# Optimization experiments

Hardware: AMD Instinct MI355X
Metric: run time of the kernel (lower is better)

The kernel has to match this reference:

```python
import jax, jax.numpy as jnp
import numpy as np

B, T, DIM, H = 4, 1024, 2048, 16
HD = DIM // H  # head_dim = 128


def _rope_tables(t, hd, theta=10000.0):
    freqs = 1.0 / (theta ** (np.arange(0, hd, 2, dtype=np.float32) / hd))  # [hd/2]
    ang = np.outer(np.arange(t, dtype=np.float32), freqs)  # [T, hd/2]
    return jnp.asarray(np.cos(ang)), jnp.asarray(np.sin(ang))


def setup_inputs() -> dict:
    key = jax.random.key(0)
    ks = jax.random.split(key, 5)
    x = jax.random.normal(ks[0], (B, T, DIM), dtype=jnp.float32)
    s = 1.0 / np.sqrt(DIM)
    wq = jax.random.normal(ks[1], (DIM, DIM), dtype=jnp.float32) * s
    wk = jax.random.normal(ks[2], (DIM, DIM), dtype=jnp.float32) * s
    wv = jax.random.normal(ks[3], (DIM, DIM), dtype=jnp.float32) * s
    wo = jax.random.normal(ks[4], (DIM, DIM), dtype=jnp.float32) * s
    freqs_cos, freqs_sin = _rope_tables(T, HD)
    return {"x": x, "freqs_cos": freqs_cos, "freqs_sin": freqs_sin,
            "wq": wq, "wk": wk, "wv": wv, "wo": wo}


def _apply_rope(t, cos, sin):
    # t: [B,T,H,HD]; cos/sin: [T,HD/2]. Adjacent feature pairs form complex numbers.
    tr = t.reshape(*t.shape[:-1], HD // 2, 2)
    te, to = tr[..., 0], tr[..., 1]
    c = cos[None, :, None, :]
    s = sin[None, :, None, :]
    oe = te * c - to * s
    oo = te * s + to * c
    return jnp.stack([oe, oo], axis=-1).reshape(t.shape)


def reference(x, freqs_cos, freqs_sin, wq, wk, wv, wo):
    # Linear layers: y = x @ W^T (torch nn.Linear convention)
    q = (x @ wq.T).reshape(B, T, H, HD)
    k = (x @ wk.T).reshape(B, T, H, HD)
    v = (x @ wv.T).reshape(B, T, H, HD)
    q = _apply_rope(q, freqs_cos, freqs_sin)
    k = _apply_rope(k, freqs_cos, freqs_sin)
    scale = 1.0 / jnp.sqrt(jnp.float32(HD))
    # non-causal SDPA (no mask in original call)
    scores = jnp.einsum('bqhd,bkhd->bhqk', q, k) * scale
    attn = jax.nn.softmax(scores, axis=-1)
    out = jnp.einsum('bhqk,bkhd->bqhd', attn, v).reshape(B, T, DIM)
    return out @ wo.T
```

## Files before the change

### kernel.cpp

```cpp
#include <hip/hip_runtime.h>
#include <stdint.h>

#define BB 4
#define TT 1024
#define DIM 2048
#define NH 16
#define HD 128
#define MR 4096
#define QKVS (3 * DIM)

typedef __attribute__((ext_vector_type(4))) float    f32x4;
typedef __attribute__((ext_vector_type(8))) uint16_t u16x8;
typedef __attribute__((ext_vector_type(4))) uint16_t u16x4;
typedef __attribute__((ext_vector_type(4))) short    s16x4;
typedef __attribute__((ext_vector_type(8))) __bf16   bf16x8;

static __device__ __forceinline__ uint16_t f2bf(float f) {
  uint32_t u = __builtin_bit_cast(uint32_t, f);
  u += 0x7fffu + ((u >> 16) & 1u);
  return (uint16_t)(u >> 16);
}
static __device__ __forceinline__ float bf2f(uint16_t b) {
  uint32_t u = ((uint32_t)b) << 16;
  return __builtin_bit_cast(float, u);
}

static __device__ __forceinline__ f32x4 mfma16(u16x8 a, u16x8 b, f32x4 c) {
  return __builtin_amdgcn_mfma_f32_16x16x32_bf16(
      __builtin_bit_cast(bf16x8, a), __builtin_bit_cast(bf16x8, b), c, 0, 0, 0);
}

static __device__ __forceinline__ void load_lds_16B(const void* g, void* l) {
  __builtin_amdgcn_global_load_lds(
      (const __attribute__((address_space(1))) void*)g,
      (__attribute__((address_space(3))) void*)l, 16, 0, 0);
}

#if defined(__has_builtin) && __has_builtin(__builtin_amdgcn_ds_read_tr16_b64_v4i16)
#define TR_BUILTIN 1
#else
#define TR_BUILTIN 0
#endif
static __device__ __forceinline__ u16x4 tr16_nw(const uint16_t* base, int byteoff) {
  __attribute__((address_space(3))) char* ap =
      (__attribute__((address_space(3))) char*)(void*)base + byteoff;
#if TR_BUILTIN
  s16x4 r = __builtin_amdgcn_ds_read_tr16_b64_v4i16(
      (__attribute__((address_space(3))) s16x4*)ap);
  return __builtin_bit_cast(u16x4, r);
#else
  u16x4 d;
  uint32_t a32 = (uint32_t)(uintptr_t)ap;
  asm volatile("ds_read_b64_tr_b16 %0, %1" : "=&v"(d) : "v"(a32));
  return d;
#endif
}
static __device__ __forceinline__ void tr_fence() {
#if !TR_BUILTIN
  asm volatile("s_waitcnt lgkmcnt(0)" ::: "memory");
  __builtin_amdgcn_sched_barrier(0);
#endif
}

__global__ __launch_bounds__(256) void cast_f32_bf16(const float* __restrict__ in,
                                                     uint16_t* __restrict__ out, int n4) {
  int i = blockIdx.x * 256 + threadIdx.x;
  if (i >= n4) return;
  f32x4 v = ((const f32x4*)in)[i];
  u16x4 o;
  o[0] = f2bf(v[0]); o[1] = f2bf(v[1]); o[2] = f2bf(v[2]); o[3] = f2bf(v[3]);
  ((u16x4*)out)[i] = o;
}

__global__ __launch_bounds__(256) void cast4_f32_bf16(const float* __restrict__ s0,
                                                      const float* __restrict__ s1,
                                                      const float* __restrict__ s2,
                                                      const float* __restrict__ s3,
                                                      uint16_t* __restrict__ out) {
  const int per = 4194304 / 4;
  int i = blockIdx.x * 256 + threadIdx.x;
  const int sel = i / per;
  const float* src = (sel == 0) ? s0 : (sel == 1) ? s1 : (sel == 2) ? s2 : s3;
  int j = i - sel * per;
  f32x4 v = ((const f32x4*)src)[j];
  u16x4 o;
  o[0] = f2bf(v[0]); o[1] = f2bf(v[1]); o[2] = f2bf(v[2]); o[3] = f2bf(v[3]);
  ((u16x4*)out)[i] = o;
}

template <int MODE>
__global__ __launch_bounds__(256) void gemm_m97(const uint16_t* __restrict__ A,
                                                const uint16_t* __restrict__ Bt,
                                                float* __restrict__ Cf,
                                                uint16_t* __restrict__ Cb,
                                                const float* __restrict__ cosT,
                                                const float* __restrict__ sinT,
                                                int M, int N, int K) {
  __shared__ __attribute__((aligned(16))) uint16_t As[128][64];
  __shared__ __attribute__((aligned(16))) uint16_t Bs[128][64];
  const int tid  = threadIdx.x;
  const int lane = tid & 63;
  const int wave = tid >> 6;
  const int lrow = lane & 15;
  const int lgrp = lane >> 4;
  const int wr   = (wave >> 1) * 64;
  const int wc   = (wave & 1) * 64;

  const int nbx = N >> 7, nby = M >> 7;
  const int nwg = nbx * nby;
  const int wg  = ((int)blockIdx.x & 7) * (nwg >> 3) + ((int)blockIdx.x >> 3);
  const long bRow = (long)(wg / nbx) << 7;
  const long bCol = (long)(wg % nbx) << 7;

  const f32x4 fz = {0.f, 0.f, 0.f, 0.f};
  f32x4 acc[4][4];
#pragma unroll
  for (int m = 0; m < 4; ++m)
#pragma unroll
    for (int n = 0; n < 4; ++n) acc[m][n] = fz;

  const int nkt = K >> 6;
  for (int kt = 0; kt < nkt; ++kt) {
    const long kb = (long)kt << 6;
    __syncthreads();
#pragma unroll
    for (int i = 0; i < 4; ++i) {
      const int L   = (i * 256 + tid) * 16;
      const int row = L >> 7;
      const int gc  = (((L >> 4) & 7) ^ (row & 7)) * 8;
      load_lds_16B(A  + (bRow + row) * (long)K + kb + gc, (char*)&As[0][0] + L);
      load_lds_16B(Bt + (bCol + row) * (long)K + kb + gc, (char*)&Bs[0][0] + L);
    }
    __syncthreads();

#pragma unroll
    for (int kk = 0; kk < 2; ++kk) {
      u16x8 af[4], bf[4];
#pragma unroll
      for (int m = 0; m < 4; ++m) {
        const int row = wr + m * 16 + lrow;
        const int ch  = (kk * 4 + lgrp) ^ (row & 7);
        af[m] = *(const u16x8*)((const char*)&As[0][0] + row * 128 + ch * 16);
      }
#pragma unroll
      for (int n = 0; n < 4; ++n) {
        const int row = wc + n * 16 + lrow;
        const int ch  = (kk * 4 + lgrp) ^ (row & 7);
        bf[n] = *(const u16x8*)((const char*)&Bs[0][0] + row * 128 + ch * 16);
      }
      __builtin_amdgcn_s_setprio(1);
#pragma unroll
      for (int m = 0; m < 4; ++m)
#pragma unroll
        for (int n = 0; n < 4; ++n) acc[m][n] = mfma16(af[m], bf[n], acc[m][n]);
      __builtin_amdgcn_s_setprio(0);
    }
  }

  const bool doRope = (MODE == 2) && (bCol < 2 * DIM);
  const bool isQ    = (MODE == 2) && (bCol < DIM);
  const float qscale = isQ ? 0.08838834764831845f : 1.0f;
#pragma unroll
  for (int m = 0; m < 4; ++m)
#pragma unroll
    for (int n = 0; n < 4; ++n) {
      const long grow0 = bRow + wr + m * 16 + lgrp * 4;
      const long gcol  = bCol + wc + n * 16 + lrow;
      if (doRope) {
        const int  fi  = ((int)gcol >> 1) & 63;
        const bool odd = (gcol & 1) != 0;
#pragma unroll
        for (int r = 0; r < 4; ++r) {
          const long grow = grow0 + r;
          const int  ttt  = (int)grow & (TT - 1);
          float v = acc[m][n][r];
          float p = __shfl_xor(v, 1, 64);
          float cc = cosT[ttt * 64 + fi];
          float ss = sinT[ttt * 64 + fi];
          float o  = odd ? (p * ss + v * cc) : (v * cc - p * ss);
          Cb[grow * (long)N + gcol] = f2bf(o * qscale);
        }
      } else {
#pragma unroll
        for (int r = 0; r < 4; ++r) {
          const long idx = (grow0 + r) * (long)N + gcol;
          if (MODE == 1) Cf[idx] = acc[m][n][r];
          else           Cb[idx] = f2bf(acc[m][n][r]);
        }
      }
    }
}

__global__ __launch_bounds__(256) void attn_fwd(const uint16_t* __restrict__ Q,
                                                const uint16_t* __restrict__ K,
                                                const uint16_t* __restrict__ V,
                                                uint16_t* __restrict__ O) {
  __shared__ __attribute__((aligned(16))) uint16_t Ks[2][64 * 128];
  __shared__ __attribute__((aligned(16))) uint16_t Vs[2][64 * 128];
  __shared__ __attribute__((aligned(16))) uint16_t Ps[4][16][72];
  const int tid  = threadIdx.x;
  const int lane = tid & 63;
  const int wave = tid >> 6;
  const int lrow = lane & 15;
  const int lgrp = lane >> 4;
  const int b  = blockIdx.x >> 4;
  const int h  = blockIdx.x & 15;
  const int qt = blockIdx.y;
  const long colBase = (long)h * HD;
  const long rs = QKVS;
  const long os = DIM;
  const long qrow0 = (long)b * TT + qt * 64 + wave * 16;

  u16x8 qf[4];
#pragma unroll
  for (int kkk = 0; kkk < 4; ++kkk)
    qf[kkk] = *(const u16x8*)(Q + (qrow0 + lrow) * rs + colBase + kkk * 32 + lgrp * 8);

  const f32x4 fz = {0.f, 0.f, 0.f, 0.f};
  f32x4 oacc[8];
#pragma unroll
  for (int nf = 0; nf < 8; ++nf) oacc[nf] = fz;
  float mst[4] = {-1e30f, -1e30f, -1e30f, -1e30f};
  float lst[4] = {0.f, 0.f, 0.f, 0.f};

  auto stage = [&](int kt, int buf) {
    const long krow = (long)b * TT + kt * 64;
#pragma unroll
    for (int i = 0; i < 4; ++i) {
      const int L = (i * 256 + tid) * 16;
      const int krw = L >> 8;
      const int ksc = ((L >> 4) & 15) ^ (krw & 7);
      load_lds_16B(K + (krow + krw) * rs + colBase + ksc * 8,
                   (char*)&Ks[buf][0] + L);
      const int vbl = L >> 11;
      const int vkv = ((L >> 7) & 15) * 4 + ((L >> 5) & 3);
      const int vd  = vbl * 16 + ((L >> 4) & 1) * 8;
      load_lds_16B(V + (krow + vkv) * rs + colBase + vd,
                   (char*)&Vs[buf][0] + L);
    }
  };

  stage(0, 0);

  for (int kt2 = 0; kt2 < TT / 64; ++kt2) {
    const int cur = kt2 & 1;
    if (kt2 < TT / 64 - 1) {
      stage(kt2 + 1, cur ^ 1);
      asm volatile("s_waitcnt vmcnt(8)" ::: "memory");
    } else {
      asm volatile("s_waitcnt vmcnt(0)" ::: "memory");
    }
    __builtin_amdgcn_s_barrier();

    f32x4 sacc[4];
#pragma unroll
    for (int n = 0; n < 4; ++n) sacc[n] = fz;
    __builtin_amdgcn_s_setprio(1);
#pragma unroll
    for (int kkk = 0; kkk < 4; ++kkk) {
#pragma unroll
      for (int n = 0; n < 4; ++n) {
        const int row = n * 16 + lrow;
        const int ch  = (kkk * 4 + lgrp) ^ (row & 7);
        u16x8 bfr = *(const u16x8*)((const char*)&Ks[cur][0] + row * 256 + ch * 16);
        sacc[n] = mfma16(qf[kkk], bfr, sacc[n]);
      }
    }
    __builtin_amdgcn_s_setprio(0);

    float pm[4];
#pragma unroll
    for (int r = 0; r < 4; ++r)
      pm[r] = fmaxf(fmaxf(sacc[0][r], sacc[1][r]), fmaxf(sacc[2][r], sacc[3][r]));
    bool need = false;
#pragma unroll
    for (int r = 0; r < 4; ++r) need = need || (pm[r] > mst[r] + 8.0f);
    if (__any(need)) {
      float rmax[4];
#pragma unroll
      for (int r = 0; r < 4; ++r) rmax[r] = pm[r];
#pragma unroll
      for (int off = 8; off >= 1; off >>= 1)
#pragma unroll
        for (int r = 0; r < 4; ++r)
          rmax[r] = fmaxf(rmax[r], __shfl_xor(rmax[r], off, 64));
#pragma unroll
      for (int r = 0; r < 4; ++r) {
        float mnew  = fmaxf(mst[r], rmax[r]);
        float alpha = __expf(mst[r] - mnew);
        mst[r] = mnew;
        lst[r] *= alpha;
#pragma unroll
        for (int nf = 0; nf < 8; ++nf) oacc[nf][r] *= alpha;
      }
    }

#pragma unroll
    for (int n = 0; n < 4; ++n)
#pragma unroll
      for (int r = 0; r < 4; ++r) {
        float pv = __expf(sacc[n][r] - mst[r]);
        lst[r] += pv;
        Ps[wave][lgrp * 4 + r][n * 16 + lrow] = f2bf(pv);
      }

    asm volatile("s_waitcnt lgkmcnt(0)" ::: "memory");

    __builtin_amdgcn_s_setprio(1);
#pragma unroll
    for (int kk2 = 0; kk2 < 2; ++kk2) {
      u16x8 af = *(const u16x8*)&Ps[wave][lrow][kk2 * 32 + lgrp * 8];
      u16x4 vlo[8], vhi[8];
#pragma unroll
      for (int nf = 0; nf < 8; ++nf) {
        const int vbase = nf * 2048 + kk2 * 1024 + lgrp * 256 + lrow * 8;
        vlo[nf] = tr16_nw(&Vs[cur][0], vbase);
        vhi[nf] = tr16_nw(&Vs[cur][0], vbase + 128);
      }
      tr_fence();
#pragma unroll
      for (int nf = 0; nf < 8; ++nf) {
        u16x8 bfr;
        bfr[0] = vlo[nf][0]; bfr[1] = vlo[nf][1];
        bfr[2] = vlo[nf][2]; bfr[3] = vlo[nf][3];
        bfr[4] = vhi[nf][0]; bfr[5] = vhi[nf][1];
        bfr[6] = vhi[nf][2]; bfr[7] = vhi[nf][3];
        oacc[nf] = mfma16(af, bfr, oacc[nf]);
      }
    }
    __builtin_amdgcn_s_setprio(0);

    __builtin_amdgcn_s_barrier();
  }

#pragma unroll
  for (int off = 8; off >= 1; off >>= 1)
#pragma unroll
    for (int r = 0; r < 4; ++r) lst[r] += __shfl_xor(lst[r], off, 64);

  float inv[4];
#pragma unroll
  for (int r = 0; r < 4; ++r) inv[r] = 1.0f / lst[r];
#pragma unroll
  for (int nf = 0; nf < 8; ++nf)
#pragma unroll
    for (int r = 0; r < 4; ++r)
      O[(qrow0 + lgrp * 4 + r) * os + colBase + nf * 16 + lrow] =
          f2bf(oacc[nf][r] * inv[r]);
}

extern "C" void kernel_launch(void* const* d_in, const int* in_sizes, int n_in,
                              void* d_out, int out_size, void* d_ws, size_t ws_size,
                              hipStream_t stream) {
  const float* x  = (const float*)d_in[0];
  const float* fc = (const float*)d_in[1];
  const float* fs = (const float*)d_in[2];
  const float* wq = (const float*)d_in[3];
  const float* wk = (const float*)d_in[4];
  const float* wv = (const float*)d_in[5];
  const float* wo = (const float*)d_in[6];
  float* out = (float*)d_out;

  uint16_t* w16  = (uint16_t*)d_ws;
  uint16_t* xb   = w16;
  uint16_t* wqkv = xb + 8388608;
  uint16_t* wob  = wqkv + 12582912;
  uint16_t* qkv  = wob + 4194304;
  uint16_t* ob   = qkv + 25165824;

  cast_f32_bf16<<<8192, 256, 0, stream>>>(x, xb, 8388608 / 4);
  cast4_f32_bf16<<<4 * 4096, 256, 0, stream>>>(wq, wk, wv, wo, wqkv);

  gemm_m97<2><<<(MR / 128) * (QKVS / 128), 256, 0, stream>>>(
      xb, wqkv, nullptr, qkv, fc, fs, MR, QKVS, DIM);

  dim3 ga(BB * NH, TT / 64);
  attn_fwd<<<ga, 256, 0, stream>>>(qkv, qkv + DIM, qkv + 2 * DIM, ob);

  gemm_m97<1><<<(MR / 128) * (DIM / 128), 256, 0, stream>>>(
      ob, wob, out, nullptr, nullptr, nullptr, MR, DIM, DIM);
}
```

Before: 263.2 us.

## Compute transposed QK^T scores and pass P through lane shuffles instead of LDS

The score MFMA now swaps its operands, so each lane holds a single query row's scores. That lets the softmax max and sum use a scalar per lane with only two cross-lane reductions. The probability tile is packed to bf16 in registers and rearranged into the A-operand layout for the PV MFMA with ds_bpermute shuffles, which removes the per-wave LDS scratch buffer and its write/read round trip. The cost is extra shuffles and selects, plus broadcasting alpha and the normalizer back to the output row layout.

```diff
diff --git a/kernel.cpp b/kernel.cpp
--- a/kernel.cpp
+++ b/kernel.cpp
@@ -12,6 +12,7 @@
 typedef __attribute__((ext_vector_type(4))) float    f32x4;
 typedef __attribute__((ext_vector_type(8))) uint16_t u16x8;
 typedef __attribute__((ext_vector_type(4))) uint16_t u16x4;
+typedef __attribute__((ext_vector_type(4))) uint32_t u32x4;
 typedef __attribute__((ext_vector_type(4))) short    s16x4;
 typedef __attribute__((ext_vector_type(8))) __bf16   bf16x8;
 
@@ -197,7 +198,6 @@
                                                 uint16_t* __restrict__ O) {
   __shared__ __attribute__((aligned(16))) uint16_t Ks[2][64 * 128];
   __shared__ __attribute__((aligned(16))) uint16_t Vs[2][64 * 128];
-  __shared__ __attribute__((aligned(16))) uint16_t Ps[4][16][72];
   const int tid  = threadIdx.x;
   const int lane = tid & 63;
   const int wave = tid >> 6;
@@ -220,8 +220,8 @@
   f32x4 oacc[8];
 #pragma unroll
   for (int nf = 0; nf < 8; ++nf) oacc[nf] = fz;
-  float mst[4] = {-1e30f, -1e30f, -1e30f, -1e30f};
-  float lst[4] = {0.f, 0.f, 0.f, 0.f};
+  float mst = -1e30f;
+  float lst = 0.f;
 
   auto stage = [&](int kt, int buf) {
     const long krow = (long)b * TT + kt * 64;
@@ -262,54 +262,68 @@
       for (int n = 0; n < 4; ++n) {
         const int row = n * 16 + lrow;
         const int ch  = (kkk * 4 + lgrp) ^ (row & 7);
-        u16x8 bfr = *(const u16x8*)((const char*)&Ks[cur][0] + row * 256 + ch * 16);
-        sacc[n] = mfma16(qf[kkk], bfr, sacc[n]);
+        u16x8 kfr = *(const u16x8*)((const char*)&Ks[cur][0] + row * 256 + ch * 16);
+        sacc[n] = mfma16(kfr, qf[kkk], sacc[n]);
       }
     }
     __builtin_amdgcn_s_setprio(0);
 
-    float pm[4];
-#pragma unroll
-    for (int r = 0; r < 4; ++r)
-      pm[r] = fmaxf(fmaxf(sacc[0][r], sacc[1][r]), fmaxf(sacc[2][r], sacc[3][r]));
-    bool need = false;
-#pragma unroll
-    for (int r = 0; r < 4; ++r) need = need || (pm[r] > mst[r] + 8.0f);
-    if (__any(need)) {
-      float rmax[4];
-#pragma unroll
-      for (int r = 0; r < 4; ++r) rmax[r] = pm[r];
-#pragma unroll
-      for (int off = 8; off >= 1; off >>= 1)
-#pragma unroll
-        for (int r = 0; r < 4; ++r)
-          rmax[r] = fmaxf(rmax[r], __shfl_xor(rmax[r], off, 64));
-#pragma unroll
-      for (int r = 0; r < 4; ++r) {
-        float mnew  = fmaxf(mst[r], rmax[r]);
-        float alpha = __expf(mst[r] - mnew);
-        mst[r] = mnew;
-        lst[r] *= alpha;
-#pragma unroll
-        for (int nf = 0; nf < 8; ++nf) oacc[nf][r] *= alpha;
-      }
-    }
-
+    float pm = sacc[0][0];
 #pragma unroll
     for (int n = 0; n < 4; ++n)
 #pragma unroll
-      for (int r = 0; r < 4; ++r) {
-        float pv = __expf(sacc[n][r] - mst[r]);
-        lst[r] += pv;
-        Ps[wave][lgrp * 4 + r][n * 16 + lrow] = f2bf(pv);
-      }
-
-    asm volatile("s_waitcnt lgkmcnt(0)" ::: "memory");
-
+      for (int r = 0; r < 4; ++r) pm = fmaxf(pm, sacc[n][r]);
+    if (__any(pm > mst + 8.0f)) {
+      float rm = pm;
+      rm = fmaxf(rm, __shfl_xor(rm, 16, 64));
+      rm = fmaxf(rm, __shfl_xor(rm, 32, 64));
+      float mnew  = fmaxf(mst, rm);
+      float alpha = __expf(mst - mnew);
+      mst = mnew;
+      lst *= alpha;
+      float aq[4];
+#pragma unroll
+      for (int r = 0; r < 4; ++r) aq[r] = __shfl(alpha, lgrp * 4 + r, 64);
+#pragma unroll
+      for (int nf = 0; nf < 8; ++nf)
+#pragma unroll
+        for (int r = 0; r < 4; ++r) oacc[nf][r] *= aq[r];
+    }
+
+    uint32_t pk[4][2];
+#pragma unroll
+    for (int n = 0; n < 4; ++n) {
+      float e0 = __expf(sacc[n][0] - mst);
+      float e1 = __expf(sacc[n][1] - mst);
+      float e2 = __expf(sacc[n][2] - mst);
+      float e3 = __expf(sacc[n][3] - mst);
+      lst += (e0 + e1) + (e2 + e3);
+      pk[n][0] = (uint32_t)f2bf(e0) | ((uint32_t)f2bf(e1) << 16);
+      pk[n][1] = (uint32_t)f2bf(e2) | ((uint32_t)f2bf(e3) << 16);
+    }
+
+    const int srcA = lrow + 32 * (lgrp & 1);
+    const int srcB = srcA + 16;
+    const bool hiB = (lgrp >> 1) != 0;
     __builtin_amdgcn_s_setprio(1);
 #pragma unroll
     for (int kk2 = 0; kk2 < 2; ++kk2) {
-      u16x8 af = *(const u16x8*)&Ps[wave][lrow][kk2 * 32 + lgrp * 8];
+      const int n0 = 2 * kk2, n1 = 2 * kk2 + 1;
+      uint32_t w0a = (uint32_t)__shfl((int)pk[n0][0], srcA, 64);
+      uint32_t w0b = (uint32_t)__shfl((int)pk[n1][0], srcA, 64);
+      uint32_t w1a = (uint32_t)__shfl((int)pk[n0][1], srcA, 64);
+      uint32_t w1b = (uint32_t)__shfl((int)pk[n1][1], srcA, 64);
+      uint32_t w2a = (uint32_t)__shfl((int)pk[n0][0], srcB, 64);
+      uint32_t w2b = (uint32_t)__shfl((int)pk[n1][0], srcB, 64);
+      uint32_t w3a = (uint32_t)__shfl((int)pk[n0][1], srcB, 64);
+      uint32_t w3b = (uint32_t)__shfl((int)pk[n1][1], srcB, 64);
+      u32x4 paw;
+      paw[0] = hiB ? w0b : w0a;
+      paw[1] = hiB ? w1b : w1a;
+      paw[2] = hiB ? w2b : w2a;
+      paw[3] = hiB ? w3b : w3a;
+      u16x8 pa = __builtin_bit_cast(u16x8, paw);
+
       u16x4 vlo[8], vhi[8];
 #pragma unroll
       for (int nf = 0; nf < 8; ++nf) {
@@ -325,7 +339,7 @@
         bfr[2] = vlo[nf][2]; bfr[3] = vlo[nf][3];
         bfr[4] = vhi[nf][0]; bfr[5] = vhi[nf][1];
         bfr[6] = vhi[nf][2]; bfr[7] = vhi[nf][3];
-        oacc[nf] = mfma16(af, bfr, oacc[nf]);
+        oacc[nf] = mfma16(pa, bfr, oacc[nf]);
       }
     }
     __builtin_amdgcn_s_setprio(0);
@@ -333,14 +347,11 @@
     __builtin_amdgcn_s_barrier();
   }
 
-#pragma unroll
-  for (int off = 8; off >= 1; off >>= 1)
-#pragma unroll
-    for (int r = 0; r < 4; ++r) lst[r] += __shfl_xor(lst[r], off, 64);
-
+  lst += __shfl_xor(lst, 16, 64);
+  lst += __shfl_xor(lst, 32, 64);
   float inv[4];
 #pragma unroll
-  for (int r = 0; r < 4; ++r) inv[r] = 1.0f / lst[r];
+  for (int r = 0; r < 4; ++r) inv[r] = 1.0f / __shfl(lst, lgrp * 4 + r, 64);
 #pragma unroll
   for (int nf = 0; nf < 8; ++nf)
 #pragma unroll
```

After: 268.6 us. +2.0%, slower.

## Replace double-buffered K/V prefetch with single-buffered synchronous staging in attention

Applied to the files above, without the earlier changes.

Drops the two-stage LDS ping-pong for K and V tiles in the attention kernel. Each iteration now issues its loads into one shared buffer and waits on __syncthreads before compute. This halves LDS use per block, which may let more blocks run per CU, but it removes the overlap between the next tile's global loads and the current tile's MFMA work. It also relies on __syncthreads producing a full vmcnt wait for the async LDS loads.

```diff
diff --git a/kernel.cpp b/kernel.cpp
--- a/kernel.cpp
+++ b/kernel.cpp
@@ -195,8 +195,8 @@
                                                 const uint16_t* __restrict__ K,
                                                 const uint16_t* __restrict__ V,
                                                 uint16_t* __restrict__ O) {
-  __shared__ __attribute__((aligned(16))) uint16_t Ks[2][64 * 128];
-  __shared__ __attribute__((aligned(16))) uint16_t Vs[2][64 * 128];
+  __shared__ __attribute__((aligned(16))) uint16_t Ks[64 * 128];
+  __shared__ __attribute__((aligned(16))) uint16_t Vs[64 * 128];
   __shared__ __attribute__((aligned(16))) uint16_t Ps[4][16][72];
   const int tid  = threadIdx.x;
   const int lane = tid & 63;
@@ -223,34 +223,21 @@
   float mst[4] = {-1e30f, -1e30f, -1e30f, -1e30f};
   float lst[4] = {0.f, 0.f, 0.f, 0.f};
 
-  auto stage = [&](int kt, int buf) {
-    const long krow = (long)b * TT + kt * 64;
+  for (int kt2 = 0; kt2 < TT / 64; ++kt2) {
+    const long krow = (long)b * TT + kt2 * 64;
+    __syncthreads();
 #pragma unroll
     for (int i = 0; i < 4; ++i) {
       const int L = (i * 256 + tid) * 16;
       const int krw = L >> 8;
       const int ksc = ((L >> 4) & 15) ^ (krw & 7);
-      load_lds_16B(K + (krow + krw) * rs + colBase + ksc * 8,
-                   (char*)&Ks[buf][0] + L);
+      load_lds_16B(K + (krow + krw) * rs + colBase + ksc * 8, (char*)Ks + L);
       const int vbl = L >> 11;
       const int vkv = ((L >> 7) & 15) * 4 + ((L >> 5) & 3);
       const int vd  = vbl * 16 + ((L >> 4) & 1) * 8;
-      load_lds_16B(V + (krow + vkv) * rs + colBase + vd,
-                   (char*)&Vs[buf][0] + L);
-    }
-  };
-
-  stage(0, 0);
-
-  for (int kt2 = 0; kt2 < TT / 64; ++kt2) {
-    const int cur = kt2 & 1;
-    if (kt2 < TT / 64 - 1) {
-      stage(kt2 + 1, cur ^ 1);
-      asm volatile("s_waitcnt vmcnt(8)" ::: "memory");
-    } else {
-      asm volatile("s_waitcnt vmcnt(0)" ::: "memory");
-    }
-    __builtin_amdgcn_s_barrier();
+      load_lds_16B(V + (krow + vkv) * rs + colBase + vd, (char*)Vs + L);
+    }
+    __syncthreads();
 
     f32x4 sacc[4];
 #pragma unroll
@@ -262,7 +249,7 @@
       for (int n = 0; n < 4; ++n) {
         const int row = n * 16 + lrow;
         const int ch  = (kkk * 4 + lgrp) ^ (row & 7);
-        u16x8 bfr = *(const u16x8*)((const char*)&Ks[cur][0] + row * 256 + ch * 16);
+        u16x8 bfr = *(const u16x8*)((const char*)Ks + row * 256 + ch * 16);
         sacc[n] = mfma16(qf[kkk], bfr, sacc[n]);
       }
     }
@@ -314,8 +301,8 @@
 #pragma unroll
       for (int nf = 0; nf < 8; ++nf) {
         const int vbase = nf * 2048 + kk2 * 1024 + lgrp * 256 + lrow * 8;
-        vlo[nf] = tr16_nw(&Vs[cur][0], vbase);
-        vhi[nf] = tr16_nw(&Vs[cur][0], vbase + 128);
+        vlo[nf] = tr16_nw(Vs, vbase);
+        vhi[nf] = tr16_nw(Vs, vbase + 128);
       }
       tr_fence();
 #pragma unroll
@@ -329,8 +316,6 @@
       }
     }
     __builtin_amdgcn_s_setprio(0);
-
-    __builtin_amdgcn_s_barrier();
   }
 
 #pragma unroll
```

New measurement: 263.7 us. About the same (+0.2%).
